# Kernel tuning notes

Hardware: AMD Instinct MI355X
Metric: run time of the kernel (lower is better)

The kernel has to match this reference:

```python
import jax, jax.numpy as jnp
import numpy as np

EMBED = 768
HEADS = 12
FACTOR = 2
LN_EPS = 1e-5


def layer_norm(x, gamma, beta):
    mu = jnp.mean(x, axis=-1, keepdims=True)
    var = jnp.mean(jnp.square(x - mu), axis=-1, keepdims=True)
    return (x - mu) * jax.lax.rsqrt(var + LN_EPS) * gamma + beta


def setup_inputs() -> dict:
    key = jax.random.key(0)
    ks = jax.random.split(key, 8)
    B, S, E = 8, 1024, EMBED
    H = FACTOR * E
    s_e = 1.0 / np.sqrt(E)
    s_h = 1.0 / np.sqrt(H)
    return {
        "x": jax.random.normal(ks[0], (B, S, E), jnp.float32),
        "Wq": jax.random.normal(ks[1], (E, E), jnp.float32) * s_e,
        "Wk": jax.random.normal(ks[2], (E, E), jnp.float32) * s_e,
        "Wv": jax.random.normal(ks[3], (E, E), jnp.float32) * s_e,
        "W1": jax.random.normal(ks[4], (E, H), jnp.float32) * s_e,
        "b1": jnp.zeros((H,), jnp.float32),
        "W2": jax.random.normal(ks[5], (H, E), jnp.float32) * s_h,
        "b2": jnp.zeros((E,), jnp.float32),
        "g1": jnp.ones((E,), jnp.float32),
        "beta1": jnp.zeros((E,), jnp.float32),
        "g2": jnp.ones((E,), jnp.float32),
        "beta2": jnp.zeros((E,), jnp.float32),
    }


def reference(x, Wq, Wk, Wv, W1, b1, W2, b2, g1, beta1, g2, beta2):
    B, S, E = x.shape
    hd = E // HEADS
    # NOTE: original reshapes (B,S,E)->(B,H,S,hd) WITHOUT transposing heads
    # (non-standard: mixes sequence blocks across heads) - replicated faithfully.
    q = (x @ Wq).reshape(B, HEADS, S, hd)
    k = (x @ Wk).reshape(B, HEADS, S, hd)
    v = (x @ Wv).reshape(B, HEADS, S, hd)
    # no 1/sqrt(d) scaling in the original
    attn = jax.nn.softmax(jnp.einsum('bnqd,bnkd->bnqk', q, k), axis=-1)
    # NOTE: original einsum 'bnqk,bnvd->bnqd' sums over BOTH k and v
    # (value is sum-pooled over its sequence axis) - replicated faithfully.
    out = jnp.einsum('bnqk,bnvd->bnqd', attn, v)
    out = out.transpose(0, 2, 1, 3).reshape(B, S, E)
    a = x + layer_norm(out, g1, beta1)
    # GELU after BOTH linears (exact GELU, torch default)
    h = jax.nn.gelu(a @ W1 + b1, approximate=False)
    m = jax.nn.gelu(h @ W2 + b2, approximate=False)
    return x + layer_norm(m, g2, beta2)
```

## Files before the change

kernel.cpp:

```cpp
#include <hip/hip_runtime.h>
#include <hip/hip_bf16.h>
#include <math.h>

#define E_ 768
#define HID_ 1536
#define SQ_ 1024

typedef unsigned short u16;
using bf16x8 = __attribute__((ext_vector_type(8))) __bf16;
using f32x4  = __attribute__((ext_vector_type(4))) float;

__device__ __forceinline__ u16 f2bf(float f) {
  union { float f; unsigned u; } v; v.f = f;
  unsigned r = v.u + 0x7FFFu + ((v.u >> 16) & 1u);
  return (u16)(r >> 16);
}
__device__ __forceinline__ float bf2f(u16 h) {
  union { unsigned u; float f; } v; v.u = ((unsigned)h) << 16; return v.f;
}
__device__ __forceinline__ float gelu_f(float x) {
  return 0.5f * x * (1.0f + erff(x * 0.70710678118654752f));
}

#define GLDS16(gp, sp) __builtin_amdgcn_global_load_lds( \
    (__attribute__((address_space(1))) const void*)(const void*)(gp), \
    (__attribute__((address_space(3))) void*)(void*)(sp), 16, 0, 0)

__global__ void prep_kernel(const float* __restrict__ x, const float* __restrict__ W1,
                            const float* __restrict__ W2, u16* __restrict__ xb,
                            u16* __restrict__ W1T, u16* __restrict__ W2T) {
  __shared__ float T[64 * 65];
  int bid = blockIdx.x, t = threadIdx.x;
  if (bid < 6144) {
    int base = bid * 1024 + t * 4;
    const float4 v = *reinterpret_cast<const float4*>(x + base);
    ushort4 o; o.x = f2bf(v.x); o.y = f2bf(v.y); o.z = f2bf(v.z); o.w = f2bf(v.w);
    *reinterpret_cast<ushort4*>(xb + base) = o;
    return;
  }
  const float* in; u16* out; int R_in, C_in, rt, ct;
  if (bid < 6432) {
    int b2 = bid - 6144; in = W1; out = W1T; R_in = 768; C_in = 1536;
    rt = b2 / 24; ct = b2 % 24;
  } else {
    int b3 = bid - 6432; in = W2; out = W2T; R_in = 1536; C_in = 768;
    rt = b3 / 12; ct = b3 % 12;
  }
  int r0 = rt << 6, c0 = ct << 6;
  int tr = t >> 4, tc4 = (t & 15) << 2;
#pragma unroll
  for (int i = 0; i < 4; ++i) {
    int row = tr + (i << 4);
    const float4 v = *reinterpret_cast<const float4*>(in + (size_t)(r0 + row) * C_in + c0 + tc4);
    T[row * 65 + tc4 + 0] = v.x;
    T[row * 65 + tc4 + 1] = v.y;
    T[row * 65 + tc4 + 2] = v.z;
    T[row * 65 + tc4 + 3] = v.w;
  }
  __syncthreads();
#pragma unroll
  for (int i = 0; i < 4; ++i) {
    int orow = tr + (i << 4);
    ushort4 o;
    o.x = f2bf(T[(tc4 + 0) * 65 + orow]);
    o.y = f2bf(T[(tc4 + 1) * 65 + orow]);
    o.z = f2bf(T[(tc4 + 2) * 65 + orow]);
    o.w = f2bf(T[(tc4 + 3) * 65 + orow]);
    *reinterpret_cast<ushort4*>(out + (size_t)(c0 + orow) * R_in + r0 + tc4) = o;
  }
}

__global__ void rowsum_kernel(const u16* __restrict__ xb, float* __restrict__ Rp) {
  int bid = blockIdx.x;
  int r = bid >> 2, c = bid & 3;
  int b = r / 12, n = r % 12;
  int t = threadIdx.x;
  int u0 = n << 10;
  int s_lo = u0 / 12;
  int s_hi = (u0 + 1023) / 12;
  int cnt = s_hi - s_lo + 1;
  int cs = s_lo + (cnt * c) / 4;
  int ce = s_lo + (cnt * (c + 1)) / 4;
  float acc[12][3];
#pragma unroll
  for (int g = 0; g < 12; ++g)
    for (int q = 0; q < 3; ++q) acc[g][q] = 0.f;
  const u16* xp = xb + (size_t)b * SQ_ * E_;
  for (int s = cs; s < ce; ++s) {
    float v0 = bf2f(xp[(size_t)s * E_ + t]);
    float v1 = bf2f(xp[(size_t)s * E_ + t + 256]);
    float v2 = bf2f(xp[(size_t)s * E_ + t + 512]);
    int du = 12 * s - u0;
#pragma unroll
    for (int g = 0; g < 12; ++g) {
      int u = du + g;
      if (u >= 0 && u < 1024) { acc[g][0] += v0; acc[g][1] += v1; acc[g][2] += v2; }
    }
  }
  float* Rr = Rp + (size_t)bid * 9216;
#pragma unroll
  for (int g = 0; g < 12; ++g) {
    Rr[g * 768 + t]       = acc[g][0];
    Rr[g * 768 + t + 256] = acc[g][1];
    Rr[g * 768 + t + 512] = acc[g][2];
  }
}

__global__ void ygemm_kernel(const float* __restrict__ Rp, const float* __restrict__ Wv,
                             float* __restrict__ P2) {
  int g = blockIdx.x, r = blockIdx.y;
  int t = threadIdx.x;
  int d = t & 63, sub = t >> 6;
  const float* R0 = Rp + (size_t)r * 4 * 9216 + g * 768;
  const float* wp = Wv + g * 64 + d;
  float a0 = 0.f, a1 = 0.f, a2 = 0.f, a3 = 0.f;
  int j0 = sub * 192;
#pragma unroll 2
  for (int jj = 0; jj < 192; jj += 4) {
    int j = j0 + jj;
    float r0v = R0[j + 0] + R0[9216 + j + 0] + R0[18432 + j + 0] + R0[27648 + j + 0];
    float r1v = R0[j + 1] + R0[9216 + j + 1] + R0[18432 + j + 1] + R0[27648 + j + 1];
    float r2v = R0[j + 2] + R0[9216 + j + 2] + R0[18432 + j + 2] + R0[27648 + j + 2];
    float r3v = R0[j + 3] + R0[9216 + j + 3] + R0[18432 + j + 3] + R0[27648 + j + 3];
    a0 += r0v * wp[(size_t)(j + 0) * 768];
    a1 += r1v * wp[(size_t)(j + 1) * 768];
    a2 += r2v * wp[(size_t)(j + 2) * 768];
    a3 += r3v * wp[(size_t)(j + 3) * 768];
  }
  __shared__ float red[256];
  red[t] = (a0 + a1) + (a2 + a3);
  __syncthreads();
  if (sub == 0)
    P2[((size_t)r * 12 + g) * 64 + d] = red[d] + red[64 + d] + red[128 + d] + red[192 + d];
}

__global__ void ln1_kernel(const float* __restrict__ P2, const float* __restrict__ g1,
                           const float* __restrict__ be1, float* __restrict__ L1) {
  int b = blockIdx.x, t = threadIdx.x;
  float y[3];
#pragma unroll
  for (int q = 0; q < 3; ++q) {
    int e = t + (q << 8);
    int n = e >> 6, d = e & 63;
    const float* Pp = P2 + ((size_t)(b * 12 + n) * 12) * 64 + d;
    float s = 0.f;
#pragma unroll
    for (int g = 0; g < 12; ++g) s += Pp[g << 6];
    y[q] = s;
  }
  float s = y[0] + y[1] + y[2];
  float sq = y[0] * y[0] + y[1] * y[1] + y[2] * y[2];
  __shared__ float red[8];
#pragma unroll
  for (int o = 32; o > 0; o >>= 1) { s += __shfl_down(s, o, 64); sq += __shfl_down(sq, o, 64); }
  if ((t & 63) == 0) { red[(t >> 6) * 2] = s; red[(t >> 6) * 2 + 1] = sq; }
  __syncthreads();
  s  = red[0] + red[2] + red[4] + red[6];
  sq = red[1] + red[3] + red[5] + red[7];
  float mu = s * (1.f / 768.f);
  float var = sq * (1.f / 768.f) - mu * mu;
  float rs = rsqrtf(var + 1e-5f);
#pragma unroll
  for (int q = 0; q < 3; ++q) {
    int e = t + (q << 8);
    L1[b * 768 + e] = (y[q] - mu) * rs * g1[e] + be1[e];
  }
}

__global__ void c1_kernel(const float* __restrict__ L1, const float* __restrict__ W1,
                          const float* __restrict__ b1, float* __restrict__ C1) {
  int bid = blockIdx.x;
  int b = bid / 48, c = bid % 48;
  int t = threadIdx.x;
  __shared__ float Ls[768];
  __shared__ float red[8][32];
  for (int q = t; q < 768; q += 256) Ls[q] = L1[b * 768 + q];
  __syncthreads();
  int tc = t & 31, ts = t >> 5;
  int n = c * 32 + tc;
  float acc = 0.f;
  int j0 = ts * 96;
#pragma unroll 4
  for (int j = j0; j < j0 + 96; ++j) acc += Ls[j] * W1[(size_t)j * HID_ + n];
  red[ts][tc] = acc;
  __syncthreads();
  if (ts == 0) {
    float s = b1[n];
#pragma unroll
    for (int k = 0; k < 8; ++k) s += red[k][tc];
    C1[b * HID_ + n] = s;
  }
}

template <int MODE>
__global__ __launch_bounds__(256, 2) void gemm_bt_kernel(
    const u16* __restrict__ A, const u16* __restrict__ BT,
    const float* __restrict__ bias, void* __restrict__ out0, void* __restrict__ out1,
    int N, int lda, int ldb) {
  __shared__ __align__(16) u16 As[128 * 64];
  __shared__ __align__(16) u16 Bs[128 * 64];
  int bid = blockIdx.x;
  int xcd = bid & 7, idx = bid >> 3;
  int mloc, n_, k_off, kk = 0;
  if (MODE == 0) { mloc = idx / 12; n_ = idx % 12; k_off = 0; }
  else           { kk = idx / 48; int rem = idx % 48; mloc = rem / 6; n_ = rem % 6; k_off = kk * 768; }
  int bm = (xcd * 8 + mloc) << 7, bn = n_ << 7;

  int t = threadIdx.x;
  int lane = t & 63, w = t >> 6;
  int wm = (w >> 1) << 6, wn = (w & 1) << 6;
  int quad = lane >> 4, l16 = lane & 15;
  f32x4 acc[4][4] = {};

  for (int k0 = 0; k0 < 768; k0 += 64) {
    __syncthreads();
#pragma unroll
    for (int i = 0; i < 4; ++i) {
      int ci = t + (i << 8);
      int r = ci >> 3, csw = ci & 7;
      int kc = csw ^ (r & 7);
      const u16* ga = A + (size_t)(bm + r) * lda + k_off + k0 + (kc << 3);
      GLDS16(ga, As + ci * 8);
      const u16* gb = BT + (size_t)(bn + r) * ldb + k_off + k0 + (kc << 3);
      GLDS16(gb, Bs + ci * 8);
    }
    __builtin_amdgcn_s_waitcnt(0);
    __syncthreads();
#pragma unroll
    for (int ks = 0; ks < 2; ++ks) {
      bf16x8 af[4], bf[4];
      int kc = (ks << 2) + quad;
#pragma unroll
      for (int mt = 0; mt < 4; ++mt) {
        int row = wm + (mt << 4) + l16;
        af[mt] = *reinterpret_cast<const bf16x8*>(As + row * 64 + ((kc ^ (row & 7)) << 3));
      }
#pragma unroll
      for (int nt = 0; nt < 4; ++nt) {
        int row = wn + (nt << 4) + l16;
        bf[nt] = *reinterpret_cast<const bf16x8*>(Bs + row * 64 + ((kc ^ (row & 7)) << 3));
      }
#pragma unroll
      for (int mt = 0; mt < 4; ++mt)
#pragma unroll
        for (int nt = 0; nt < 4; ++nt)
          acc[mt][nt] = __builtin_amdgcn_mfma_f32_16x16x32_bf16(af[mt], bf[nt], acc[mt][nt], 0, 0, 0);
    }
  }

#pragma unroll
  for (int mt = 0; mt < 4; ++mt) {
    int row0 = bm + wm + (mt << 4) + (quad << 2);
#pragma unroll
    for (int nt = 0; nt < 4; ++nt) {
      int col = bn + wn + (nt << 4) + l16;
      float bv = (MODE == 0) ? bias[(bm >> 10) * N + col] : 0.f;
#pragma unroll
      for (int rr = 0; rr < 4; ++rr) {
        float v = acc[mt][nt][rr] + bv;
        size_t idxo = (size_t)(row0 + rr) * N + col;
        if (MODE == 0)       ((u16*)out0)[idxo] = f2bf(gelu_f(v));
        else if (kk == 0)    ((float*)out0)[idxo] = v;
        else                 ((u16*)out1)[idxo] = f2bf(v);
      }
    }
  }
}

__global__ void ln2_kernel(const float* __restrict__ p0, const u16* __restrict__ p1,
                           const float* __restrict__ x, const float* __restrict__ b2,
                           const float* __restrict__ g2, const float* __restrict__ be2,
                           float* __restrict__ out) {
  int row = blockIdx.x, t = threadIdx.x;
  const float* pr = p0 + (size_t)row * 768;
  const u16* qr = p1 + (size_t)row * 768;
  float v0 = gelu_f(pr[t]       + bf2f(qr[t])       + b2[t]);
  float v1 = gelu_f(pr[t + 256] + bf2f(qr[t + 256]) + b2[t + 256]);
  float v2 = gelu_f(pr[t + 512] + bf2f(qr[t + 512]) + b2[t + 512]);
  float s = v0 + v1 + v2;
  float sq = v0 * v0 + v1 * v1 + v2 * v2;
  __shared__ float red[8];
#pragma unroll
  for (int o = 32; o > 0; o >>= 1) { s += __shfl_down(s, o, 64); sq += __shfl_down(sq, o, 64); }
  if ((t & 63) == 0) { red[(t >> 6) * 2] = s; red[(t >> 6) * 2 + 1] = sq; }
  __syncthreads();
  s  = red[0] + red[2] + red[4] + red[6];
  sq = red[1] + red[3] + red[5] + red[7];
  float mu = s * (1.f / 768.f);
  float var = sq * (1.f / 768.f) - mu * mu;
  float rs = rsqrtf(var + 1e-5f);
  const float* xr = x + (size_t)row * 768;
  float* orow = out + (size_t)row * 768;
  orow[t]       = xr[t]       + (v0 - mu) * rs * g2[t]       + be2[t];
  orow[t + 256] = xr[t + 256] + (v1 - mu) * rs * g2[t + 256] + be2[t + 256];
  orow[t + 512] = xr[t + 512] + (v2 - mu) * rs * g2[t + 512] + be2[t + 512];
}

extern "C" void kernel_launch(void* const* d_in, const int* in_sizes, int n_in,
                              void* d_out, int out_size, void* d_ws, size_t ws_size,
                              hipStream_t stream) {
  const float* x   = (const float*)d_in[0];
  const float* Wv  = (const float*)d_in[3];
  const float* W1  = (const float*)d_in[4];
  const float* b1  = (const float*)d_in[5];
  const float* W2  = (const float*)d_in[6];
  const float* b2  = (const float*)d_in[7];
  const float* g1  = (const float*)d_in[8];
  const float* be1 = (const float*)d_in[9];
  const float* g2  = (const float*)d_in[10];
  const float* be2 = (const float*)d_in[11];
  float* out = (float*)d_out;

  char* ws = (char*)d_ws;
  u16*   xb  = (u16*)(ws);
  u16*   W1T = (u16*)(ws + 12582912);
  u16*   W2T = (u16*)(ws + 14942208);
  u16*   h   = (u16*)(ws + 17301504);
  float* Rp  = (float*)(ws + 17301504);
  float* P2  = (float*)(ws + 42467328);
  float* L1  = (float*)(ws + 42762240);
  float* C1  = (float*)(ws + 42786816);
  u16*   p1  = xb;

  prep_kernel<<<6720, 256, 0, stream>>>(x, W1, W2, xb, W1T, W2T);
  rowsum_kernel<<<384, 256, 0, stream>>>(xb, Rp);
  ygemm_kernel<<<dim3(12, 96), 256, 0, stream>>>(Rp, Wv, P2);
  ln1_kernel<<<8, 256, 0, stream>>>(P2, g1, be1, L1);
  c1_kernel<<<384, 256, 0, stream>>>(L1, W1, b1, C1);
  gemm_bt_kernel<0><<<768, 256, 0, stream>>>(xb, W1T, C1, (void*)h, nullptr, 1536, 768, 768);
  gemm_bt_kernel<1><<<768, 256, 0, stream>>>(h, W2T, nullptr, (void*)out, (void*)p1, 768, 1536, 1536);
  ln2_kernel<<<8192, 256, 0, stream>>>(out, p1, x, b2, g2, be2, out);
}
```

Before: 242.0 us.

## Split ygemm reduction over eight j-chunks and store split-K GEMM partial as bf16

The ygemm kernel now launches an extra grid dimension of 8 chunks, each covering 96 of the 768 reduction indices. Partial sums go to a larger P3 buffer that ln1 sums over 96 entries per element. This raises parallelism in a kernel that previously launched only 1152 blocks, each running a long serial loop. Separately, the first split-K partial of the second GEMM is written as bf16 to a new workspace buffer instead of fp32 into the output, which halves that traffic but loses precision before the final GELU and layer norm.

```diff
diff --git a/kernel.cpp b/kernel.cpp
--- a/kernel.cpp
+++ b/kernel.cpp
@@ -107,16 +107,16 @@
 }
 
 __global__ void ygemm_kernel(const float* __restrict__ Rp, const float* __restrict__ Wv,
-                             float* __restrict__ P2) {
-  int g = blockIdx.x, r = blockIdx.y;
+                             float* __restrict__ P3) {
+  int g = blockIdx.x, r = blockIdx.y, jc = blockIdx.z;
   int t = threadIdx.x;
   int d = t & 63, sub = t >> 6;
   const float* R0 = Rp + (size_t)r * 4 * 9216 + g * 768;
   const float* wp = Wv + g * 64 + d;
+  int j0 = jc * 96 + sub * 24;
   float a0 = 0.f, a1 = 0.f, a2 = 0.f, a3 = 0.f;
-  int j0 = sub * 192;
-#pragma unroll 2
-  for (int jj = 0; jj < 192; jj += 4) {
+#pragma unroll
+  for (int jj = 0; jj < 24; jj += 4) {
     int j = j0 + jj;
     float r0v = R0[j + 0] + R0[9216 + j + 0] + R0[18432 + j + 0] + R0[27648 + j + 0];
     float r1v = R0[j + 1] + R0[9216 + j + 1] + R0[18432 + j + 1] + R0[27648 + j + 1];
@@ -131,10 +131,10 @@
   red[t] = (a0 + a1) + (a2 + a3);
   __syncthreads();
   if (sub == 0)
-    P2[((size_t)r * 12 + g) * 64 + d] = red[d] + red[64 + d] + red[128 + d] + red[192 + d];
-}
-
-__global__ void ln1_kernel(const float* __restrict__ P2, const float* __restrict__ g1,
+    P3[(((size_t)r * 12 + g) * 8 + jc) * 64 + d] = red[d] + red[64 + d] + red[128 + d] + red[192 + d];
+}
+
+__global__ void ln1_kernel(const float* __restrict__ P3, const float* __restrict__ g1,
                            const float* __restrict__ be1, float* __restrict__ L1) {
   int b = blockIdx.x, t = threadIdx.x;
   float y[3];
@@ -142,10 +142,10 @@
   for (int q = 0; q < 3; ++q) {
     int e = t + (q << 8);
     int n = e >> 6, d = e & 63;
-    const float* Pp = P2 + ((size_t)(b * 12 + n) * 12) * 64 + d;
+    const float* Pp = P3 + (size_t)(b * 12 + n) * 96 * 64 + d;
     float s = 0.f;
-#pragma unroll
-    for (int g = 0; g < 12; ++g) s += Pp[g << 6];
+#pragma unroll 8
+    for (int gj = 0; gj < 96; ++gj) s += Pp[gj << 6];
     y[q] = s;
   }
   float s = y[0] + y[1] + y[2];
@@ -260,23 +260,23 @@
         float v = acc[mt][nt][rr] + bv;
         size_t idxo = (size_t)(row0 + rr) * N + col;
         if (MODE == 0)       ((u16*)out0)[idxo] = f2bf(gelu_f(v));
-        else if (kk == 0)    ((float*)out0)[idxo] = v;
+        else if (kk == 0)    ((u16*)out0)[idxo] = f2bf(v);
         else                 ((u16*)out1)[idxo] = f2bf(v);
       }
     }
   }
 }
 
-__global__ void ln2_kernel(const float* __restrict__ p0, const u16* __restrict__ p1,
+__global__ void ln2_kernel(const u16* __restrict__ p0, const u16* __restrict__ p1,
                            const float* __restrict__ x, const float* __restrict__ b2,
                            const float* __restrict__ g2, const float* __restrict__ be2,
                            float* __restrict__ out) {
   int row = blockIdx.x, t = threadIdx.x;
-  const float* pr = p0 + (size_t)row * 768;
+  const u16* pr = p0 + (size_t)row * 768;
   const u16* qr = p1 + (size_t)row * 768;
-  float v0 = gelu_f(pr[t]       + bf2f(qr[t])       + b2[t]);
-  float v1 = gelu_f(pr[t + 256] + bf2f(qr[t + 256]) + b2[t + 256]);
-  float v2 = gelu_f(pr[t + 512] + bf2f(qr[t + 512]) + b2[t + 512]);
+  float v0 = gelu_f(bf2f(pr[t])       + bf2f(qr[t])       + b2[t]);
+  float v1 = gelu_f(bf2f(pr[t + 256]) + bf2f(qr[t + 256]) + b2[t + 256]);
+  float v2 = gelu_f(bf2f(pr[t + 512]) + bf2f(qr[t + 512]) + b2[t + 512]);
   float s = v0 + v1 + v2;
   float sq = v0 * v0 + v1 * v1 + v2 * v2;
   __shared__ float red[8];
@@ -317,17 +317,18 @@
   u16*   W2T = (u16*)(ws + 14942208);
   u16*   h   = (u16*)(ws + 17301504);
   float* Rp  = (float*)(ws + 17301504);
-  float* P2  = (float*)(ws + 42467328);
-  float* L1  = (float*)(ws + 42762240);
-  float* C1  = (float*)(ws + 42786816);
+  float* P3  = (float*)(ws + 42467328);
+  float* L1  = (float*)(ws + 44826624);
+  float* C1  = (float*)(ws + 44851200);
+  u16*   m0  = (u16*)(ws + 44900352);
   u16*   p1  = xb;
 
   prep_kernel<<<6720, 256, 0, stream>>>(x, W1, W2, xb, W1T, W2T);
   rowsum_kernel<<<384, 256, 0, stream>>>(xb, Rp);
-  ygemm_kernel<<<dim3(12, 96), 256, 0, stream>>>(Rp, Wv, P2);
-  ln1_kernel<<<8, 256, 0, stream>>>(P2, g1, be1, L1);
+  ygemm_kernel<<<dim3(12, 96, 8), 256, 0, stream>>>(Rp, Wv, P3);
+  ln1_kernel<<<8, 256, 0, stream>>>(P3, g1, be1, L1);
   c1_kernel<<<384, 256, 0, stream>>>(L1, W1, b1, C1);
   gemm_bt_kernel<0><<<768, 256, 0, stream>>>(xb, W1T, C1, (void*)h, nullptr, 1536, 768, 768);
-  gemm_bt_kernel<1><<<768, 256, 0, stream>>>(h, W2T, nullptr, (void*)out, (void*)p1, 768, 1536, 1536);
-  ln2_kernel<<<8192, 256, 0, stream>>>(out, p1, x, b2, g2, be2, out);
-}
+  gemm_bt_kernel<1><<<768, 256, 0, stream>>>(h, W2T, nullptr, (void*)m0, (void*)p1, 768, 1536, 1536);
+  ln2_kernel<<<8192, 256, 0, stream>>>(m0, p1, x, b2, g2, be2, out);
+}
```

Measured after the change: 252.5 us. 1.04x slower.
